# Kernel optimization log

Hardware: AMD Instinct MI355X
Metric: run time of the kernel (lower is better)

Reference implementation:

```python
import jax, jax.numpy as jnp
import numpy as np

N_NODES = 100000
N_EDGES = 1600000
IN_DIM, HID_DIM, OUT_DIM = 128, 256, 128


def gcn_conv(x, edge_index, W, b):
    """PyG GCNConv: add self-loops, sym-normalize, linear transform, scatter-add, bias."""
    n = x.shape[0]
    loop = jnp.arange(n, dtype=edge_index.dtype)
    src = jnp.concatenate([edge_index[0], loop])  # message source (x_j)
    dst = jnp.concatenate([edge_index[1], loop])  # aggregation target
    deg = jax.ops.segment_sum(jnp.ones_like(dst, dtype=x.dtype), dst, num_segments=n)
    dinv = jnp.where(deg > 0, deg ** -0.5, 0.0).astype(x.dtype)
    norm = dinv[src] * dinv[dst]                  # [E+N]
    h = x @ W                                     # [N, out]
    msg = h[src] * norm[:, None]                  # [E+N, out] gather
    out = jax.ops.segment_sum(msg, dst, num_segments=n)  # scatter-add
    return out + b


def setup_inputs() -> dict:
    key = jax.random.key(0)
    k = jax.random.split(key, 6)
    x = jax.random.normal(k[0], (N_NODES, IN_DIM), dtype=jnp.float32)
    edge_index = jax.random.randint(k[1], (2, N_EDGES), 0, N_NODES, dtype=jnp.int64)
    # Glorot-ish init for weights
    W1 = jax.random.normal(k[2], (IN_DIM, HID_DIM), dtype=jnp.float32) * (1.0 / np.sqrt(IN_DIM))
    b1 = jnp.zeros((HID_DIM,), dtype=jnp.float32)
    W2 = jax.random.normal(k[3], (HID_DIM, OUT_DIM), dtype=jnp.float32) * (1.0 / np.sqrt(HID_DIM))
    b2 = jnp.zeros((OUT_DIM,), dtype=jnp.float32)
    return {"x": x, "edge_index": edge_index, "W1": W1, "b1": b1, "W2": W2, "b2": b2}


def reference(x, edge_index, W1, b1, W2, b2):
    h = gcn_conv(x, edge_index, W1, b1)
    h = jax.nn.relu(h)  # relu between layers (drop_rate=0 -> no dropout)
    h = gcn_conv(h, edge_index, W2, b2)
    return h
```

## Files before the change

### kernel.cpp

```cpp
#include <hip/hip_runtime.h>
#include <hip/hip_bf16.h>

#define N_NODES 100000
#define N_EDGES 1600000
#define IN_DIM 128
#define HID_DIM 256
#define OUT_DIM 128
#define NB ((N_NODES + 1023) / 1024)
#define DCHUNK 12500
#define EGRID 8192
#define CAP 64
#define NSTRIP (N_NODES / 16)
#define GWAVES 2048

#define FILLB 8192
#define FPREP 258
#define FCONVX 12500
#define FUSED_TOTAL (FILLB + FPREP + FCONVX)

#define PB_ZERO 391
#define PB_PREP 258
#define PB_CONVX 12500
#define PB_TOTAL (PB_ZERO + PB_PREP + PB_CONVX)

typedef __attribute__((ext_vector_type(8))) short bf16x8;
typedef __attribute__((ext_vector_type(4))) float f32x4;
typedef __attribute__((ext_vector_type(4))) float float4v;
typedef unsigned long long ull;
typedef unsigned short u16;

__device__ __forceinline__ float bf2f(u16 u) {
  union { unsigned int i; float f; } c; c.i = ((unsigned int)u) << 16; return c.f;
}
__device__ __forceinline__ u16 f2bf(float f) {
  __hip_bfloat16 h = __float2bfloat16(f);
  return *(u16*)&h;
}

__global__ void detect_zero_kernel(const int* __restrict__ ei,
                                   const unsigned int* __restrict__ xw,
                                   int* __restrict__ flags, int* __restrict__ cnt) {
  int tid = threadIdx.x;
  int i = blockIdx.x * 256 + tid;
  if (i < N_NODES) cnt[i] = 0;
  if (blockIdx.x == 0 && tid < 64) {
    const long long* p = (const long long*)ei;
    long long v = p[tid & 15];
    int ebad = (tid < 16) && (v < 0 || v >= N_NODES);
    ull ebm = __ballot(ebad);
    int isf32 = 0;
    #pragma unroll
    for (int k = 0; k < 4; ++k) {
      unsigned int ex = (xw[tid * 4 + k] >> 7) & 0xFF;
      if (ex >= 0xC0) isf32 = 1;
    }
    ull fbm = __ballot(isf32);
    if (tid == 0) {
      flags[0] = (ebm == 0) ? 1 : 0;
      flags[1] = (fbm != 0) ? 1 : 0;
    }
  }
}

__device__ __forceinline__ int edge_at(const int* ei, int idx, int mode) {
  return mode ? (int)((const long long*)ei)[idx] : ei[idx];
}

__global__ void fill_prep_kernel(const int* __restrict__ ei, const void* __restrict__ x,
                                 const void* __restrict__ W1, const void* __restrict__ b1,
                                 const void* __restrict__ W2, const void* __restrict__ b2,
                                 const int* __restrict__ flags,
                                 int* __restrict__ cnt, int* __restrict__ csrf,
                                 u16* __restrict__ Wt1, u16* __restrict__ Wt2,
                                 u16* __restrict__ b1c, u16* __restrict__ b2c,
                                 u16* __restrict__ xc) {
  int b = blockIdx.x, tid = threadIdx.x;
  if (b < FILLB) {
    int g = b & 7;
    unsigned lo = (unsigned)(g * DCHUNK);
    unsigned hi = lo + DCHUNK; if (hi > N_NODES) hi = N_NODES;
    int stride = (FILLB >> 3) * 256;
    int e0 = (b >> 3) * 256 + tid;
    if (flags[0]) {
      const long long* s64 = (const long long*)ei;
      const long long* d64 = s64 + N_EDGES;
      for (int e = e0; e < N_EDGES; e += stride) {
        unsigned d = (unsigned)(int)d64[e];
        if (d >= lo && d < hi) {
          int s = (int)s64[e];
          int p = atomicAdd(&cnt[d], 1);
          if (p < CAP) csrf[d * CAP + p] = s;
        }
      }
    } else {
      const int* d32 = ei + N_EDGES;
      for (int e = e0; e < N_EDGES; e += stride) {
        unsigned d = (unsigned)d32[e];
        if (d >= lo && d < hi) {
          int s = ei[e];
          int p = atomicAdd(&cnt[d], 1);
          if (p < CAP) csrf[d * CAP + p] = s;
        }
      }
    }
  } else if (b < FILLB + FPREP) {
    int i = (b - FILLB) * 256 + tid;
    int f = flags[1];
    auto cvt = [&](const void* P, int idx) -> u16 {
      return f ? f2bf(((const float*)P)[idx]) : ((const u16*)P)[idx];
    };
    if (i < 32768) {
      int k = i >> 8, n = i & 255;
      Wt1[n * 128 + k] = cvt(W1, i);
    } else if (i < 65536) {
      int j = i - 32768;
      int k = j >> 7, n = j & 127;
      Wt2[n * 256 + k] = cvt(W2, j);
    } else if (i < 65792) {
      b1c[i - 65536] = cvt(b1, i - 65536);
    } else if (i < 65920) {
      b2c[i - 65792] = cvt(b2, i - 65792);
    }
  } else {
    int i = (b - FILLB - FPREP) * 256 + tid;
    if (i >= N_NODES * IN_DIM / 4) return;
    if (flags[1]) {
      float4v v = ((const float4v*)x)[i];
      ull w = (ull)f2bf(v.x) | ((ull)f2bf(v.y) << 16) | ((ull)f2bf(v.z) << 32) |
              ((ull)f2bf(v.w) << 48);
      ((ull*)xc)[i] = w;
    } else {
      ((ull*)xc)[i] = ((const ull*)x)[i];
    }
  }
}

__global__ void degnorm_kernel(const int* __restrict__ cnt, float* __restrict__ dinv) {
  int i = blockIdx.x * 256 + threadIdx.x;
  if (i < N_NODES) dinv[i] = rsqrtf((float)(cnt[i] + 1));
}

__global__ void zero_kernel(int* p, int n) {
  int i = blockIdx.x * 256 + threadIdx.x;
  if (i < n) p[i] = 0;
}

__global__ void prologue_kernel(const void* __restrict__ x,
                                const void* __restrict__ W1, const void* __restrict__ b1,
                                const void* __restrict__ W2, const void* __restrict__ b2,
                                const int* __restrict__ flags,
                                int* __restrict__ cnt,
                                u16* __restrict__ Wt1, u16* __restrict__ Wt2,
                                u16* __restrict__ b1c, u16* __restrict__ b2c,
                                u16* __restrict__ xc) {
  int b = blockIdx.x, tid = threadIdx.x;
  if (b < PB_ZERO) {
    int i = b * 256 + tid;
    if (i < N_NODES) cnt[i] = 0;
  } else if (b < PB_ZERO + PB_PREP) {
    int i = (b - PB_ZERO) * 256 + tid;
    int f = flags[1];
    auto cvt = [&](const void* P, int idx) -> u16 {
      return f ? f2bf(((const float*)P)[idx]) : ((const u16*)P)[idx];
    };
    if (i < 32768) {
      int k = i >> 8, n = i & 255;
      Wt1[n * 128 + k] = cvt(W1, i);
    } else if (i < 65536) {
      int j = i - 32768;
      int k = j >> 7, n = j & 127;
      Wt2[n * 256 + k] = cvt(W2, j);
    } else if (i < 65792) {
      b1c[i - 65536] = cvt(b1, i - 65536);
    } else if (i < 65920) {
      b2c[i - 65792] = cvt(b2, i - 65792);
    }
  } else {
    int i = (b - PB_ZERO - PB_PREP) * 256 + tid;
    if (i >= N_NODES * IN_DIM / 4) return;
    if (flags[1]) {
      float4v v = ((const float4v*)x)[i];
      ull w = (ull)f2bf(v.x) | ((ull)f2bf(v.y) << 16) | ((ull)f2bf(v.z) << 32) |
              ((ull)f2bf(v.w) << 48);
      ((ull*)xc)[i] = w;
    } else {
      ((ull*)xc)[i] = ((const ull*)x)[i];
    }
  }
}

__global__ void count_kernel(const int* __restrict__ ei, const int* __restrict__ flags,
                             int* __restrict__ deg) {
  int g = blockIdx.x & 7;
  unsigned lo = (unsigned)(g * DCHUNK);
  unsigned hi = lo + DCHUNK; if (hi > N_NODES) hi = N_NODES;
  int m = flags[0];
  int stride = (EGRID >> 3) * 256;
  for (int e = (blockIdx.x >> 3) * 256 + threadIdx.x; e < N_EDGES; e += stride) {
    unsigned d = (unsigned)edge_at(ei, N_EDGES + e, m);
    if (d >= lo && d < hi) atomicAdd(&deg[d], 1);
  }
}

__global__ __launch_bounds__(1024) void bsum_kernel(const int* __restrict__ deg,
                                                    int* __restrict__ bsum, int n) {
  __shared__ int ws[16];
  int tid = threadIdx.x, lane = tid & 63, wid = tid >> 6;
  int idx = blockIdx.x * 1024 + tid;
  int v = (idx < n) ? deg[idx] : 0;
  #pragma unroll
  for (int o = 32; o > 0; o >>= 1) v += __shfl_down(v, o);
  if (lane == 0) ws[wid] = v;
  __syncthreads();
  if (tid == 0) {
    int r = 0;
    #pragma unroll
    for (int i = 0; i < 16; ++i) r += ws[i];
    bsum[blockIdx.x] = r;
  }
}

__global__ void bscan_kernel(const int* __restrict__ bsum, int* __restrict__ boff,
                             int* __restrict__ total, int nb) {
  int lane = threadIdx.x;
  int carry = 0;
  for (int c = 0; c < (nb + 63) / 64; ++c) {
    int idx = c * 64 + lane;
    int v = (idx < nb) ? bsum[idx] : 0;
    int x = v;
    #pragma unroll
    for (int o = 1; o < 64; o <<= 1) {
      int y = __shfl_up(x, o);
      if (lane >= o) x += y;
    }
    if (idx < nb) boff[idx] = carry + x - v;
    carry += __shfl(x, 63);
  }
  if (lane == 0) *total = carry;
}

__global__ __launch_bounds__(1024) void bfill_kernel(const int* __restrict__ deg,
                                                     const int* __restrict__ boff,
                                                     int* __restrict__ off,
                                                     int* __restrict__ cur,
                                                     float* __restrict__ dinv, int n) {
  __shared__ int wsum[16];
  __shared__ int wpre[16];
  int tid = threadIdx.x, lane = tid & 63, wid = tid >> 6;
  int idx = blockIdx.x * 1024 + tid;
  int v = (idx < n) ? deg[idx] : 0;
  int x = v;
  #pragma unroll
  for (int o = 1; o < 64; o <<= 1) {
    int y = __shfl_up(x, o);
    if (lane >= o) x += y;
  }
  if (lane == 63) wsum[wid] = x;
  __syncthreads();
  if (tid == 0) {
    int r = 0;
    #pragma unroll
    for (int i = 0; i < 16; ++i) { wpre[i] = r; r += wsum[i]; }
  }
  __syncthreads();
  int excl = boff[blockIdx.x] + wpre[wid] + x - v;
  if (idx < n) {
    off[idx] = excl;
    cur[idx] = excl;
    dinv[idx] = rsqrtf((float)(v + 1));
  }
}

__global__ void fill_kernel(const int* __restrict__ ei, const int* __restrict__ flags,
                            int* __restrict__ cur, int* __restrict__ csr) {
  int g = blockIdx.x & 7;
  unsigned lo = (unsigned)(g * DCHUNK);
  unsigned hi = lo + DCHUNK; if (hi > N_NODES) hi = N_NODES;
  int m = flags[0];
  int stride = (EGRID >> 3) * 256;
  for (int e = (blockIdx.x >> 3) * 256 + threadIdx.x; e < N_EDGES; e += stride) {
    unsigned d = (unsigned)edge_at(ei, N_EDGES + e, m);
    if (d >= lo && d < hi) {
      int s = edge_at(ei, e, m);
      int p = atomicAdd(&cur[d], 1);
      if ((unsigned)p < N_EDGES) csr[p] = s;
    }
  }
}

template <bool BIAS, bool OUTF32, bool FIXED>
__global__ __launch_bounds__(256) void agg_kernel(
    const u16* __restrict__ V, const int* __restrict__ off,
    const int* __restrict__ csr, const float* __restrict__ dinv,
    const u16* __restrict__ bias, void* __restrict__ outv) {
  int d = (blockIdx.x * 256 + threadIdx.x) >> 6;
  int lane = threadIdx.x & 63;
  if (d >= N_NODES) return;
  int du = __builtin_amdgcn_readfirstlane(d);
  int grp = lane >> 4, sub = lane & 15;
  float dv = dinv[du];
  bf16x8 w0 = *(const bf16x8*)(V + (size_t)du * 128 + sub * 8);
  float self_s = (grp == 0) ? dv : 0.0f;
  float a[8];
  #pragma unroll
  for (int k = 0; k < 8; ++k) a[k] = self_s * bf2f((u16)w0[k]);
  int e, e1;
  if (FIXED) {
    int c = __builtin_amdgcn_readfirstlane(off[du]);
    if (c > CAP) c = CAP;
    e = du * CAP;
    e1 = e + c;
  } else {
    e  = __builtin_amdgcn_readfirstlane(off[du]);
    e1 = __builtin_amdgcn_readfirstlane(off[du + 1]);
  }
  for (; e + 8 <= e1; e += 8) {
    int sA = csr[e + grp];
    int sB = csr[e + 4 + grp];
    float dsA = dinv[sA];
    float dsB = dinv[sB];
    bf16x8 wA = *(const bf16x8*)(V + (size_t)sA * 128 + sub * 8);
    bf16x8 wB = *(const bf16x8*)(V + (size_t)sB * 128 + sub * 8);
    #pragma unroll
    for (int k = 0; k < 8; ++k) a[k] = fmaf(dsA, bf2f((u16)wA[k]), a[k]);
    #pragma unroll
    for (int k = 0; k < 8; ++k) a[k] = fmaf(dsB, bf2f((u16)wB[k]), a[k]);
  }
  for (; e + 4 <= e1; e += 4) {
    int s = csr[e + grp];
    float ds = dinv[s];
    bf16x8 w = *(const bf16x8*)(V + (size_t)s * 128 + sub * 8);
    #pragma unroll
    for (int k = 0; k < 8; ++k) a[k] = fmaf(ds, bf2f((u16)w[k]), a[k]);
  }
  int rem = e1 - e;
  if (rem > 0) {
    int ee = e + (grp < rem ? grp : 0);
    int s = csr[ee];
    float ds = (grp < rem) ? dinv[s] : 0.0f;
    bf16x8 w = *(const bf16x8*)(V + (size_t)s * 128 + sub * 8);
    #pragma unroll
    for (int k = 0; k < 8; ++k) a[k] = fmaf(ds, bf2f((u16)w[k]), a[k]);
  }
  #pragma unroll
  for (int k = 0; k < 8; ++k) {
    a[k] += __shfl_xor(a[k], 16);
    a[k] += __shfl_xor(a[k], 32);
    a[k] *= dv;
  }
  if (BIAS) {
    bf16x8 bv = *(const bf16x8*)(bias + sub * 8);
    #pragma unroll
    for (int k = 0; k < 8; ++k) a[k] += bf2f((u16)bv[k]);
  }
  if (OUTF32) {
    if (grp < 2) {
      f32x4 o4;
      #pragma unroll
      for (int r = 0; r < 4; ++r) o4[r] = a[grp * 4 + r];
      *(f32x4*)((float*)outv + (size_t)du * 128 + sub * 8 + grp * 4) = o4;
    }
  } else {
    if (grp == 0) {
      bf16x8 ob;
      #pragma unroll
      for (int k = 0; k < 8; ++k) ob[k] = (short)f2bf(a[k]);
      *(bf16x8*)((u16*)outv + (size_t)du * 128 + sub * 8) = ob;
    }
  }
}

__global__ __launch_bounds__(256) void mlp1_kernel(
    const u16* __restrict__ xa, const u16* __restrict__ Wt1,
    const u16* __restrict__ b1, u16* __restrict__ h) {
  __shared__ u16 B[32768];
  int tid = threadIdx.x;
  #pragma unroll
  for (int j = 0; j < 16; ++j) {
    int i = j * 256 + tid;
    int row = i >> 4, blk = i & 15;
    int phys = (row << 4) | (blk ^ (row & 15));
    *(bf16x8*)&B[phys * 8] = *(const bf16x8*)(Wt1 + (size_t)i * 8);
  }
  __syncthreads();
  int wid = tid >> 6, lane = tid & 63, ml = lane & 15, q = lane >> 4;
  for (int s = blockIdx.x * 4 + wid; s < NSTRIP; s += GWAVES) {
    const short* Ar = (const short*)xa + (size_t)(s * 16 + ml) * IN_DIM + q * 8;
    f32x4 acc[16] = {};
    #pragma unroll
    for (int k0 = 0; k0 < IN_DIM; k0 += 32) {
      bf16x8 a = *(const bf16x8*)(Ar + k0);
      int kb = k0 >> 3;
      #pragma unroll
      for (int t = 0; t < 16; ++t) {
        int brow = t * 16 + ml;
        const u16* Bp = &B[(((unsigned)brow << 4) | (unsigned)((kb + q) ^ ml)) * 8];
        acc[t] = __builtin_amdgcn_mfma_f32_16x16x32_bf16(a, *(const bf16x8*)Bp, acc[t], 0, 0, 0);
      }
    }
    size_t hb = (size_t)s * 16 * HID_DIM;
    #pragma unroll
    for (int t = 0; t < 16; ++t) {
      float bv = bf2f(b1[t * 16 + ml]);
      #pragma unroll
      for (int r = 0; r < 4; ++r)
        h[hb + (size_t)(q * 4 + r) * HID_DIM + t * 16 + ml] =
            f2bf(fmaxf(acc[t][r] + bv, 0.0f));
    }
  }
}

__global__ __launch_bounds__(256) void mlp2_kernel(
    const u16* __restrict__ h, const u16* __restrict__ Wt2, u16* __restrict__ xg) {
  __shared__ u16 B[32768];
  int tid = threadIdx.x;
  #pragma unroll
  for (int j = 0; j < 16; ++j) {
    int i = j * 256 + tid;
    int row = i >> 5, blk = i & 31;
    int phys = (row << 5) | (blk ^ (row & 15));
    *(bf16x8*)&B[phys * 8] = *(const bf16x8*)(Wt2 + (size_t)i * 8);
  }
  __syncthreads();
  int wid = tid >> 6, lane = tid & 63, ml = lane & 15, q = lane >> 4;
  for (int s = blockIdx.x * 4 + wid; s < NSTRIP; s += GWAVES) {
    const short* Ar = (const short*)h + (size_t)(s * 16 + ml) * HID_DIM + q * 8;
    f32x4 acc[8] = {};
    #pragma unroll
    for (int k0 = 0; k0 < HID_DIM; k0 += 32) {
      bf16x8 a = *(const bf16x8*)(Ar + k0);
      int kb = k0 >> 3;
      #pragma unroll
      for (int t = 0; t < 8; ++t) {
        int brow = t * 16 + ml;
        const u16* Bp = &B[(((unsigned)brow << 5) | (unsigned)((kb + q) ^ ml)) * 8];
        acc[t] = __builtin_amdgcn_mfma_f32_16x16x32_bf16(a, *(const bf16x8*)Bp, acc[t], 0, 0, 0);
      }
    }
    size_t gb = (size_t)s * 16 * OUT_DIM;
    #pragma unroll
    for (int t = 0; t < 8; ++t) {
      #pragma unroll
      for (int r = 0; r < 4; ++r)
        xg[gb + (size_t)(q * 4 + r) * OUT_DIM + t * 16 + ml] = f2bf(acc[t][r]);
    }
  }
}

extern "C" void kernel_launch(void* const* d_in, const int* in_sizes, int n_in,
                              void* d_out, int out_size, void* d_ws, size_t ws_size,
                              hipStream_t stream) {
  const void* x  = d_in[0];
  const int*  ei = (const int*)d_in[1];
  const void* W1 = d_in[2];
  const void* b1 = d_in[3];
  const void* W2 = d_in[4];
  const void* b2 = d_in[5];

  char* wsb = (char*)d_ws;

  {
    size_t o = 0;
    auto carve = [&](size_t bytes) {
      o = (o + 511) & ~(size_t)511;
      void* p = wsb + o;
      o += bytes;
      return p;
    };
    int*   flags = (int*)carve(8);
    int*   cnt  = (int*)carve((size_t)N_NODES * 4);
    float* dinv = (float*)carve((size_t)N_NODES * 4);
    int*   csrf = (int*)carve((size_t)N_NODES * CAP * 4);
    u16*   Wt1 = (u16*)carve((size_t)IN_DIM * HID_DIM * 2);
    u16*   Wt2 = (u16*)carve((size_t)HID_DIM * OUT_DIM * 2);
    u16*   b1c = (u16*)carve((size_t)HID_DIM * 2);
    u16*   b2c = (u16*)carve((size_t)OUT_DIM * 2);
    u16*   xc  = (u16*)carve((size_t)N_NODES * 128 * 2);
    u16*   xa  = (u16*)carve((size_t)N_NODES * 128 * 2);
    u16*   h   = (u16*)d_out;
    if (o <= ws_size) {
      detect_zero_kernel<<<391, 256, 0, stream>>>(ei, (const unsigned int*)x, flags, cnt);
      fill_prep_kernel<<<FUSED_TOTAL, 256, 0, stream>>>(ei, x, W1, b1, W2, b2, flags,
                                                        cnt, csrf, Wt1, Wt2, b1c, b2c, xc);
      degnorm_kernel<<<(N_NODES + 255) / 256, 256, 0, stream>>>(cnt, dinv);
      agg_kernel<false, false, true>
          <<<(N_NODES * 64) / 256, 256, 0, stream>>>(xc, cnt, csrf, dinv, nullptr, xa);
      mlp1_kernel<<<512, 256, 0, stream>>>(xa, Wt1, b1c, h);
      mlp2_kernel<<<512, 256, 0, stream>>>(h, Wt2, xa);
      agg_kernel<true, true, true>
          <<<(N_NODES * 64) / 256, 256, 0, stream>>>(xa, cnt, csrf, dinv, b2c, d_out);
      return;
    }
  }

  size_t o = 0;
  auto carve = [&](size_t bytes) {
    o = (o + 511) & ~(size_t)511;
    void* p = wsb + o;
    o += bytes;
    return p;
  };
  int*   flags = (int*)carve(8);
  int*   deg  = (int*)carve((size_t)N_NODES * 4);
  int*   off  = (int*)carve((size_t)(N_NODES + 1) * 4);
  int*   cur  = (int*)carve((size_t)N_NODES * 4);
  float* dinv = (float*)carve((size_t)N_NODES * 4);
  int*   csr  = (int*)carve((size_t)N_EDGES * 4);
  int*   bsum = (int*)carve((size_t)NB * 4);
  int*   boff = (int*)carve((size_t)NB * 4);
  u16*   Wt1 = (u16*)carve((size_t)IN_DIM * HID_DIM * 2);
  u16*   Wt2 = (u16*)carve((size_t)HID_DIM * OUT_DIM * 2);
  u16*   b1c = (u16*)carve((size_t)HID_DIM * 2);
  u16*   b2c = (u16*)carve((size_t)OUT_DIM * 2);
  u16*   xc  = (u16*)carve((size_t)N_NODES * 128 * 2);
  u16*   xa  = (u16*)carve((size_t)N_NODES * 128 * 2);
  u16*   h   = (u16*)d_out;

  detect_zero_kernel<<<391, 256, 0, stream>>>(ei, (const unsigned int*)x, flags, deg);
  prologue_kernel<<<PB_TOTAL, 256, 0, stream>>>(x, W1, b1, W2, b2, flags,
                                                deg, Wt1, Wt2, b1c, b2c, xc);
  count_kernel<<<EGRID, 256, 0, stream>>>(ei, flags, deg);
  bsum_kernel<<<NB, 1024, 0, stream>>>(deg, bsum, N_NODES);
  bscan_kernel<<<1, 64, 0, stream>>>(bsum, boff, off + N_NODES, NB);
  bfill_kernel<<<NB, 1024, 0, stream>>>(deg, boff, off, cur, dinv, N_NODES);
  fill_kernel<<<EGRID, 256, 0, stream>>>(ei, flags, cur, csr);

  agg_kernel<false, false, false>
      <<<(N_NODES * 64) / 256, 256, 0, stream>>>(xc, off, csr, dinv, nullptr, xa);
  mlp1_kernel<<<512, 256, 0, stream>>>(xa, Wt1, b1c, h);
  mlp2_kernel<<<512, 256, 0, stream>>>(h, Wt2, xa);
  agg_kernel<true, true, false>
      <<<(N_NODES * 64) / 256, 256, 0, stream>>>(xa, off, csr, dinv, b2c, d_out);
}
```

Before: 349.5 us.

## Prescale layer-2 features by dinv in GEMM epilogue and batch neighbor index loads via shuffles

```diff
diff --git a/kernel.cpp b/kernel.cpp
--- a/kernel.cpp
+++ b/kernel.cpp
@@ -13,10 +13,10 @@
 #define NSTRIP (N_NODES / 16)
 #define GWAVES 2048
 
+#define FCONVX 12500
+#define FPREP 258
 #define FILLB 8192
-#define FPREP 258
-#define FCONVX 12500
-#define FUSED_TOTAL (FILLB + FPREP + FCONVX)
+#define FUSED_TOTAL (FCONVX + FPREP + FILLB)
 
 #define PB_ZERO 391
 #define PB_PREP 258
@@ -75,12 +75,42 @@
                                  u16* __restrict__ b1c, u16* __restrict__ b2c,
                                  u16* __restrict__ xc) {
   int b = blockIdx.x, tid = threadIdx.x;
-  if (b < FILLB) {
-    int g = b & 7;
+  if (b < FCONVX) {
+    int i = b * 256 + tid;
+    if (i >= N_NODES * IN_DIM / 4) return;
+    if (flags[1]) {
+      float4v v = ((const float4v*)x)[i];
+      ull w = (ull)f2bf(v.x) | ((ull)f2bf(v.y) << 16) | ((ull)f2bf(v.z) << 32) |
+              ((ull)f2bf(v.w) << 48);
+      ((ull*)xc)[i] = w;
+    } else {
+      ((ull*)xc)[i] = ((const ull*)x)[i];
+    }
+  } else if (b < FCONVX + FPREP) {
+    int i = (b - FCONVX) * 256 + tid;
+    int f = flags[1];
+    auto cvt = [&](const void* P, int idx) -> u16 {
+      return f ? f2bf(((const float*)P)[idx]) : ((const u16*)P)[idx];
+    };
+    if (i < 32768) {
+      int k = i >> 8, n = i & 255;
+      Wt1[n * 128 + k] = cvt(W1, i);
+    } else if (i < 65536) {
+      int j = i - 32768;
+      int k = j >> 7, n = j & 127;
+      Wt2[n * 256 + k] = cvt(W2, j);
+    } else if (i < 65792) {
+      b1c[i - 65536] = cvt(b1, i - 65536);
+    } else if (i < 65920) {
+      b2c[i - 65792] = cvt(b2, i - 65792);
+    }
+  } else {
+    int fb = b - FCONVX - FPREP;
+    int g = fb & 7;
     unsigned lo = (unsigned)(g * DCHUNK);
     unsigned hi = lo + DCHUNK; if (hi > N_NODES) hi = N_NODES;
     int stride = (FILLB >> 3) * 256;
-    int e0 = (b >> 3) * 256 + tid;
+    int e0 = (fb >> 3) * 256 + tid;
     if (flags[0]) {
       const long long* s64 = (const long long*)ei;
       const long long* d64 = s64 + N_EDGES;
@@ -103,46 +133,12 @@
         }
       }
     }
-  } else if (b < FILLB + FPREP) {
-    int i = (b - FILLB) * 256 + tid;
-    int f = flags[1];
-    auto cvt = [&](const void* P, int idx) -> u16 {
-      return f ? f2bf(((const float*)P)[idx]) : ((const u16*)P)[idx];
-    };
-    if (i < 32768) {
-      int k = i >> 8, n = i & 255;
-      Wt1[n * 128 + k] = cvt(W1, i);
-    } else if (i < 65536) {
-      int j = i - 32768;
-      int k = j >> 7, n = j & 127;
-      Wt2[n * 256 + k] = cvt(W2, j);
-    } else if (i < 65792) {
-      b1c[i - 65536] = cvt(b1, i - 65536);
-    } else if (i < 65920) {
-      b2c[i - 65792] = cvt(b2, i - 65792);
-    }
-  } else {
-    int i = (b - FILLB - FPREP) * 256 + tid;
-    if (i >= N_NODES * IN_DIM / 4) return;
-    if (flags[1]) {
-      float4v v = ((const float4v*)x)[i];
-      ull w = (ull)f2bf(v.x) | ((ull)f2bf(v.y) << 16) | ((ull)f2bf(v.z) << 32) |
-              ((ull)f2bf(v.w) << 48);
-      ((ull*)xc)[i] = w;
-    } else {
-      ((ull*)xc)[i] = ((const ull*)x)[i];
-    }
   }
 }
 
 __global__ void degnorm_kernel(const int* __restrict__ cnt, float* __restrict__ dinv) {
   int i = blockIdx.x * 256 + threadIdx.x;
   if (i < N_NODES) dinv[i] = rsqrtf((float)(cnt[i] + 1));
-}
-
-__global__ void zero_kernel(int* p, int n) {
-  int i = blockIdx.x * 256 + threadIdx.x;
-  if (i < n) p[i] = 0;
 }
 
 __global__ void prologue_kernel(const void* __restrict__ x,
@@ -288,7 +284,7 @@
   }
 }
 
-template <bool BIAS, bool OUTF32, bool FIXED>
+template <bool BIAS, bool OUTF32, bool FIXED, bool PRESCALED>
 __global__ __launch_bounds__(256) void agg_kernel(
     const u16* __restrict__ V, const int* __restrict__ off,
     const int* __restrict__ csr, const float* __restrict__ dinv,
@@ -300,47 +296,60 @@
   int grp = lane >> 4, sub = lane & 15;
   float dv = dinv[du];
   bf16x8 w0 = *(const bf16x8*)(V + (size_t)du * 128 + sub * 8);
-  float self_s = (grp == 0) ? dv : 0.0f;
+  float self_s = (grp == 0) ? (PRESCALED ? 1.0f : dv) : 0.0f;
   float a[8];
   #pragma unroll
   for (int k = 0; k < 8; ++k) a[k] = self_s * bf2f((u16)w0[k]);
-  int e, e1;
+
   if (FIXED) {
     int c = __builtin_amdgcn_readfirstlane(off[du]);
     if (c > CAP) c = CAP;
-    e = du * CAP;
-    e1 = e + c;
+    int sj = csr[du * CAP + (lane < c ? lane : 0)];
+    if ((unsigned)sj >= N_NODES) sj = 0;
+    float dj;
+    if (PRESCALED) dj = (lane < c) ? 1.0f : 0.0f;
+    else           dj = (lane < c) ? dinv[sj] : 0.0f;
+    int nit = (c + 3) >> 2;
+    int t = 0;
+    for (; t + 2 <= nit; t += 2) {
+      int jA = 4 * t + grp, jB = jA + 4;
+      int sA = __shfl(sj, jA), sB = __shfl(sj, jB);
+      float dsA = __shfl(dj, jA);
+      float dsB = __shfl(dj, jB);
+      bf16x8 wA = *(const bf16x8*)(V + (size_t)sA * 128 + sub * 8);
+      bf16x8 wB = *(const bf16x8*)(V + (size_t)sB * 128 + sub * 8);
+      #pragma unroll
+      for (int k = 0; k < 8; ++k) a[k] = fmaf(dsA, bf2f((u16)wA[k]), a[k]);
+      #pragma unroll
+      for (int k = 0; k < 8; ++k) a[k] = fmaf(dsB, bf2f((u16)wB[k]), a[k]);
+    }
+    if (t < nit) {
+      int j = 4 * t + grp;
+      int s = __shfl(sj, j);
+      float ds = __shfl(dj, j);
+      bf16x8 w = *(const bf16x8*)(V + (size_t)s * 128 + sub * 8);
+      #pragma unroll
+      for (int k = 0; k < 8; ++k) a[k] = fmaf(ds, bf2f((u16)w[k]), a[k]);
+    }
   } else {
-    e  = __builtin_amdgcn_readfirstlane(off[du]);
-    e1 = __builtin_amdgcn_readfirstlane(off[du + 1]);
-  }
-  for (; e + 8 <= e1; e += 8) {
-    int sA = csr[e + grp];
-    int sB = csr[e + 4 + grp];
-    float dsA = dinv[sA];
-    float dsB = dinv[sB];
-    bf16x8 wA = *(const bf16x8*)(V + (size_t)sA * 128 + sub * 8);
-    bf16x8 wB = *(const bf16x8*)(V + (size_t)sB * 128 + sub * 8);
-    #pragma unroll
-    for (int k = 0; k < 8; ++k) a[k] = fmaf(dsA, bf2f((u16)wA[k]), a[k]);
-    #pragma unroll
-    for (int k = 0; k < 8; ++k) a[k] = fmaf(dsB, bf2f((u16)wB[k]), a[k]);
-  }
-  for (; e + 4 <= e1; e += 4) {
-    int s = csr[e + grp];
-    float ds = dinv[s];
-    bf16x8 w = *(const bf16x8*)(V + (size_t)s * 128 + sub * 8);
-    #pragma unroll
-    for (int k = 0; k < 8; ++k) a[k] = fmaf(ds, bf2f((u16)w[k]), a[k]);
-  }
-  int rem = e1 - e;
-  if (rem > 0) {
-    int ee = e + (grp < rem ? grp : 0);
-    int s = csr[ee];
-    float ds = (grp < rem) ? dinv[s] : 0.0f;
-    bf16x8 w = *(const bf16x8*)(V + (size_t)s * 128 + sub * 8);
-    #pragma unroll
-    for (int k = 0; k < 8; ++k) a[k] = fmaf(ds, bf2f((u16)w[k]), a[k]);
+    int e  = __builtin_amdgcn_readfirstlane(off[du]);
+    int e1 = __builtin_amdgcn_readfirstlane(off[du + 1]);
+    for (; e + 4 <= e1; e += 4) {
+      int s = csr[e + grp];
+      float ds = PRESCALED ? 1.0f : dinv[s];
+      bf16x8 w = *(const bf16x8*)(V + (size_t)s * 128 + sub * 8);
+      #pragma unroll
+      for (int k = 0; k < 8; ++k) a[k] = fmaf(ds, bf2f((u16)w[k]), a[k]);
+    }
+    int rem = e1 - e;
+    if (rem > 0) {
+      int ee = e + (grp < rem ? grp : 0);
+      int s = csr[ee];
+      float ds = (grp < rem) ? (PRESCALED ? 1.0f : dinv[s]) : 0.0f;
+      bf16x8 w = *(const bf16x8*)(V + (size_t)s * 128 + sub * 8);
+      #pragma unroll
+      for (int k = 0; k < 8; ++k) a[k] = fmaf(ds, bf2f((u16)w[k]), a[k]);
+    }
   }
   #pragma unroll
   for (int k = 0; k < 8; ++k) {
@@ -411,7 +420,8 @@
 }
 
 __global__ __launch_bounds__(256) void mlp2_kernel(
-    const u16* __restrict__ h, const u16* __restrict__ Wt2, u16* __restrict__ xg) {
+    const u16* __restrict__ h, const u16* __restrict__ Wt2,
+    const float* __restrict__ dinv, u16* __restrict__ xg) {
   __shared__ u16 B[32768];
   int tid = threadIdx.x;
   #pragma unroll
@@ -437,12 +447,13 @@
         acc[t] = __builtin_amdgcn_mfma_f32_16x16x32_bf16(a, *(const bf16x8*)Bp, acc[t], 0, 0, 0);
       }
     }
+    f32x4 dv4 = *(const f32x4*)(dinv + (size_t)s * 16 + q * 4);
     size_t gb = (size_t)s * 16 * OUT_DIM;
     #pragma unroll
     for (int t = 0; t < 8; ++t) {
       #pragma unroll
       for (int r = 0; r < 4; ++r)
-        xg[gb + (size_t)(q * 4 + r) * OUT_DIM + t * 16 + ml] = f2bf(acc[t][r]);
+        xg[gb + (size_t)(q * 4 + r) * OUT_DIM + t * 16 + ml] = f2bf(acc[t][r] * dv4[r]);
     }
   }
 }
@@ -483,11 +494,11 @@
       fill_prep_kernel<<<FUSED_TOTAL, 256, 0, stream>>>(ei, x, W1, b1, W2, b2, flags,
                                                         cnt, csrf, Wt1, Wt2, b1c, b2c, xc);
       degnorm_kernel<<<(N_NODES + 255) / 256, 256, 0, stream>>>(cnt, dinv);
-      agg_kernel<false, false, true>
+      agg_kernel<false, false, true, false>
           <<<(N_NODES * 64) / 256, 256, 0, stream>>>(xc, cnt, csrf, dinv, nullptr, xa);
       mlp1_kernel<<<512, 256, 0, stream>>>(xa, Wt1, b1c, h);
-      mlp2_kernel<<<512, 256, 0, stream>>>(h, Wt2, xa);
-      agg_kernel<true, true, true>
+      mlp2_kernel<<<512, 256, 0, stream>>>(h, Wt2, dinv, xa);
+      agg_kernel<true, true, true, true>
           <<<(N_NODES * 64) / 256, 256, 0, stream>>>(xa, cnt, csrf, dinv, b2c, d_out);
       return;
     }
@@ -525,10 +536,10 @@
   bfill_kernel<<<NB, 1024, 0, stream>>>(deg, boff, off, cur, dinv, N_NODES);
   fill_kernel<<<EGRID, 256, 0, stream>>>(ei, flags, cur, csr);
 
-  agg_kernel<false, false, false>
+  agg_kernel<false, false, false, false>
       <<<(N_NODES * 64) / 256, 256, 0, stream>>>(xc, off, csr, dinv, nullptr, xa);
   mlp1_kernel<<<512, 256, 0, stream>>>(xa, Wt1, b1c, h);
-  mlp2_kernel<<<512, 256, 0, stream>>>(h, Wt2, xa);
-  agg_kernel<true, true, false>
+  mlp2_kernel<<<512, 256, 0, stream>>>(h, Wt2, dinv, xa);
+  agg_kernel<true, true, false, true>
       <<<(N_NODES * 64) / 256, 256, 0, stream>>>(xa, off, csr, dinv, b2c, d_out);
 }
```

Result: no change. 353.8 us (+1.2%).
